# Kernel tuning notes

Measured on AMD Instinct MI355X. Metric: run time of the kernel, lower is better.

## Reference

```python
import math
import jax, jax.numpy as jnp
import numpy as np

B, T, D, H = 1, 4096, 1024, 16
HD = D // H  # 64

def setup_inputs() -> dict:
    key = jax.random.key(0)
    k1, k2, k3 = jax.random.split(key, 3)
    x = jax.random.normal(k1, (B, T, D), dtype=jnp.float32)
    # torch nn.Linear weight layout: [out_features, in_features]
    w_attn = jax.random.normal(k2, (3 * D, D), dtype=jnp.float32) * (1.0 / math.sqrt(D))
    w_proj = jax.random.normal(k3, (D, D), dtype=jnp.float32) * (1.0 / math.sqrt(D))
    return {"x": x, "w_attn": w_attn, "w_proj": w_proj}

def reference(x, w_attn, w_proj):
    b, t, d = x.shape
    qkv = jnp.einsum('btd,ed->bte', x, w_attn)  # [B,T,3D]
    q, k, v = jnp.split(qkv, 3, axis=-1)
    # [B,H,T,HD]
    q = q.reshape(b, t, H, HD).transpose(0, 2, 1, 3)
    k = k.reshape(b, t, H, HD).transpose(0, 2, 1, 3)
    v = v.reshape(b, t, H, HD).transpose(0, 2, 1, 3)
    scale = 1.0 / math.sqrt(HD)
    att = jnp.einsum('bhqd,bhkd->bhqk', q, k) * scale  # [B,H,T,T]
    causal = jnp.tril(jnp.ones((t, t), dtype=bool))
    att = jnp.where(causal[None, None], att, -jnp.inf)
    att = jax.nn.softmax(att, axis=-1)
    y = jnp.einsum('bhqk,bhkd->bhqd', att, v)  # [B,H,T,HD]
    y = y.transpose(0, 2, 1, 3).reshape(b, t, d)
    return jnp.einsum('btd,ed->bte', y, w_proj)
```

## Files before the change

### kernel.cpp

```cpp
#include <hip/hip_runtime.h>
#include <hip/hip_bf16.h>

typedef __bf16 bf16x8 __attribute__((ext_vector_type(8)));
typedef float  f32x4  __attribute__((ext_vector_type(4)));
typedef short  sh4    __attribute__((ext_vector_type(4)));

__device__ __forceinline__ void async_load16(const void* g, void* l) {
    __builtin_amdgcn_global_load_lds(
        (const __attribute__((address_space(1))) unsigned int*)g,
        (__attribute__((address_space(3))) unsigned int*)l,
        16, 0, 0);
}

__device__ __forceinline__ bool sniff_is_bf16(const void* src) {
    const unsigned int* p = (const unsigned int*)src;
    unsigned v = p[threadIdx.x & 63];
    unsigned e = (v >> 7) & 0xFF;
    unsigned long long m = __ballot(e >= 100 && e <= 140);
    return __popcll(m) >= 48;
}

__global__ __launch_bounds__(256) void to_bf16(const void* __restrict__ src,
                                               __bf16* __restrict__ dst, int n) {
    bool b16 = sniff_is_bf16(src);
    int i = (blockIdx.x * 256 + threadIdx.x) * 4;
    if (i >= n) return;
    if (b16) {
        *(uint2*)(dst + i) = *(const uint2*)((const __bf16*)src + i);
    } else {
        float4 v = *(const float4*)((const float*)src + i);
        dst[i]     = (__bf16)v.x;
        dst[i + 1] = (__bf16)v.y;
        dst[i + 2] = (__bf16)v.z;
        dst[i + 3] = (__bf16)v.w;
    }
}

__global__ __launch_bounds__(256) void gemm_bt(
    const __bf16* __restrict__ A,
    const __bf16* __restrict__ B,
    void* __restrict__ Cv,
    int M, int N, int K,
    const void* sniff)
{
    bool out_b16 = true;
    if (sniff) out_b16 = sniff_is_bf16(sniff);

    __shared__ __bf16 As[3 * 128 * 32];
    __shared__ __bf16 Bs[3 * 128 * 32];

    const int nwg = gridDim.x;
    const int cpx = nwg >> 3;
    const int sid = (blockIdx.x & 7) * cpx + (blockIdx.x >> 3);
    const int nbx = N >> 7;
    const int bx  = sid % nbx;
    const int by  = sid / nbx;

    const int tid  = threadIdx.x;
    const int lane = tid & 63;
    const int w    = tid >> 6;
    const int wm   = w >> 1, wn = w & 1;
    const int m0   = by * 128;
    const int n0   = bx * 128;
    const int c    = lane & 15;
    const int g    = lane >> 4;

    f32x4 acc[4][4] = {};

    const int e0 = tid * 8;
    const int e1 = e0 + 2048;
    const int r0 = e0 >> 5, c0 = e0 & 31;
    const int r1 = e1 >> 5, c1 = e1 & 31;

    const __bf16* a0 = A + (size_t)(m0 + r0) * K + c0;
    const __bf16* a1 = A + (size_t)(m0 + r1) * K + c1;
    const __bf16* b0 = B + (size_t)(n0 + r0) * K + c0;
    const __bf16* b1 = B + (size_t)(n0 + r1) * K + c1;

    const int KT = K >> 5;

    async_load16(a0, As + e0);
    async_load16(a1, As + e1);
    async_load16(b0, Bs + e0);
    async_load16(b1, Bs + e1);
    async_load16(a0 + 32, As + 4096 + e0);
    async_load16(a1 + 32, As + 4096 + e1);
    async_load16(b0 + 32, Bs + 4096 + e0);
    async_load16(b1 + 32, Bs + 4096 + e1);

    int cb = 0, sb = 2;
    for (int kt = 0; kt < KT; ++kt) {
        if (kt + 1 < KT) asm volatile("s_waitcnt vmcnt(4)" ::: "memory");
        else             asm volatile("s_waitcnt vmcnt(0)" ::: "memory");
        __builtin_amdgcn_s_barrier();
        asm volatile("" ::: "memory");

        if (kt + 2 < KT) {
            const int k0 = (kt + 2) << 5;
            async_load16(a0 + k0, As + sb * 4096 + e0);
            async_load16(a1 + k0, As + sb * 4096 + e1);
            async_load16(b0 + k0, Bs + sb * 4096 + e0);
            async_load16(b1 + k0, Bs + sb * 4096 + e1);
        }

        const __bf16* as_ = As + cb * 4096;
        const __bf16* bs_ = Bs + cb * 4096;

        bf16x8 af[4], bfr[4];
        #pragma unroll
        for (int i = 0; i < 4; i++)
            af[i] = *(const bf16x8*)&as_[(wm * 64 + i * 16 + c) * 32 + g * 8];
        #pragma unroll
        for (int j = 0; j < 4; j++)
            bfr[j] = *(const bf16x8*)&bs_[(wn * 64 + j * 16 + c) * 32 + g * 8];
        #pragma unroll
        for (int i = 0; i < 4; i++)
            #pragma unroll
            for (int j = 0; j < 4; j++)
                acc[i][j] = __builtin_amdgcn_mfma_f32_16x16x32_bf16(af[i], bfr[j], acc[i][j], 0, 0, 0);

        cb = (cb == 2) ? 0 : cb + 1;
        sb = (sb == 2) ? 0 : sb + 1;
    }

    #pragma unroll
    for (int i = 0; i < 4; i++) {
        const int row0 = m0 + wm * 64 + i * 16 + g * 4;
        #pragma unroll
        for (int j = 0; j < 4; j++) {
            const int col = n0 + wn * 64 + j * 16 + c;
            #pragma unroll
            for (int r = 0; r < 4; r++) {
                const size_t idx = (size_t)(row0 + r) * N + col;
                if (out_b16) ((__bf16*)Cv)[idx] = (__bf16)acc[i][j][r];
                else         ((float*)Cv)[idx]  = acc[i][j][r];
            }
        }
    }
}

__global__ __launch_bounds__(256) void gemm_bt64(
    const __bf16* __restrict__ A,
    const __bf16* __restrict__ B,
    void* __restrict__ Cv,
    int M, int N, int K,
    const void* sniff)
{
    bool out_b16 = true;
    if (sniff) out_b16 = sniff_is_bf16(sniff);

    __shared__ __bf16 As[3 * 128 * 32];
    __shared__ __bf16 Bs[3 * 64 * 32];

    const int nwg = gridDim.x;
    const int cpx = nwg >> 3;
    const int sid = (blockIdx.x & 7) * cpx + (blockIdx.x >> 3);
    const int nbx = N >> 6;
    const int bx  = sid % nbx;
    const int by  = sid / nbx;

    const int tid  = threadIdx.x;
    const int lane = tid & 63;
    const int w    = tid >> 6;
    const int wm   = w >> 1, wn = w & 1;
    const int m0   = by * 128;
    const int n0   = bx * 64;
    const int c    = lane & 15;
    const int g    = lane >> 4;

    f32x4 acc[4][2] = {};

    const int e0 = tid * 8;
    const int e1 = e0 + 2048;
    const int r0 = e0 >> 5, c0 = e0 & 31;
    const int r1 = e1 >> 5, c1 = e1 & 31;
    const int rb = tid >> 2, cbk = (tid & 3) * 8;

    const __bf16* a0 = A + (size_t)(m0 + r0) * K + c0;
    const __bf16* a1 = A + (size_t)(m0 + r1) * K + c1;
    const __bf16* bp = B + (size_t)(n0 + rb) * K + cbk;

    const int KT = K >> 5;

    async_load16(a0, As + e0);
    async_load16(a1, As + e1);
    async_load16(bp, Bs + e0);
    async_load16(a0 + 32, As + 4096 + e0);
    async_load16(a1 + 32, As + 4096 + e1);
    async_load16(bp + 32, Bs + 2048 + e0);

    int cb = 0, sb = 2;
    for (int kt = 0; kt < KT; ++kt) {
        if (kt + 1 < KT) asm volatile("s_waitcnt vmcnt(3)" ::: "memory");
        else             asm volatile("s_waitcnt vmcnt(0)" ::: "memory");
        __builtin_amdgcn_s_barrier();
        asm volatile("" ::: "memory");

        if (kt + 2 < KT) {
            const int k0 = (kt + 2) << 5;
            async_load16(a0 + k0, As + sb * 4096 + e0);
            async_load16(a1 + k0, As + sb * 4096 + e1);
            async_load16(bp + k0, Bs + sb * 2048 + e0);
        }

        const __bf16* as_ = As + cb * 4096;
        const __bf16* bs_ = Bs + cb * 2048;

        bf16x8 af[4], bfr[2];
        #pragma unroll
        for (int i = 0; i < 4; i++)
            af[i] = *(const bf16x8*)&as_[(wm * 64 + i * 16 + c) * 32 + g * 8];
        #pragma unroll
        for (int j = 0; j < 2; j++)
            bfr[j] = *(const bf16x8*)&bs_[(wn * 32 + j * 16 + c) * 32 + g * 8];
        #pragma unroll
        for (int i = 0; i < 4; i++)
            #pragma unroll
            for (int j = 0; j < 2; j++)
                acc[i][j] = __builtin_amdgcn_mfma_f32_16x16x32_bf16(af[i], bfr[j], acc[i][j], 0, 0, 0);

        cb = (cb == 2) ? 0 : cb + 1;
        sb = (sb == 2) ? 0 : sb + 1;
    }

    #pragma unroll
    for (int i = 0; i < 4; i++) {
        const int row0 = m0 + wm * 64 + i * 16 + g * 4;
        #pragma unroll
        for (int j = 0; j < 2; j++) {
            const int col = n0 + wn * 32 + j * 16 + c;
            #pragma unroll
            for (int r = 0; r < 4; r++) {
                const size_t idx = (size_t)(row0 + r) * N + col;
                if (out_b16) ((__bf16*)Cv)[idx] = (__bf16)acc[i][j][r];
                else         ((float*)Cv)[idx]  = acc[i][j][r];
            }
        }
    }
}

__global__ __launch_bounds__(256) void vtrans(const __bf16* __restrict__ qkv,
                                              __bf16* __restrict__ vT) {
    __shared__ __bf16 Lt[64 * 72];
    const int tid = threadIdx.x;
    const int h   = blockIdx.y;
    const int t0  = blockIdx.x * 64;
    #pragma unroll
    for (int rr = 0; rr < 2; rr++) {
        int e = rr * 2048 + tid * 8;
        int tr = e >> 6, tc = e & 63;
        bf16x8 v = *(const bf16x8*)&qkv[(size_t)(t0 + tr) * 3072 + 2048 + h * 64 + tc];
        #pragma unroll
        for (int i = 0; i < 8; i++) Lt[(tc + i) * 72 + tr] = v[i];
    }
    __syncthreads();
    #pragma unroll
    for (int rr = 0; rr < 2; rr++) {
        int e = rr * 2048 + tid * 8;
        int dr = e >> 6, dc = e & 63;
        *(bf16x8*)&vT[(size_t)h * 262144 + (size_t)dr * 4096 + t0 + dc]
            = *(const bf16x8*)&Lt[dr * 72 + dc];
    }
}

__global__ __launch_bounds__(512, 4) void attn_fwd(
    const __bf16* __restrict__ qkv,
    const __bf16* __restrict__ vT,
    __bf16* __restrict__ y)
{
    constexpr int LDQ = 3072;
    constexpr float SCL = 0.18033688011112042f;

    __shared__ __align__(16) char raw[50176];
    __bf16* ksb = (__bf16*)raw;
    __bf16* vsb = (__bf16*)(raw + 24576);
    float*  ls  = (float*)(raw + 49152);
    float*  F   = (float*)raw;

    const int id   = blockIdx.x;
    const int h    = (id & 7) * 2 + (id >> 8);
    const int pr   = (id >> 3) & 31;
    const int tid  = threadIdx.x;
    const int lane = tid & 63;
    const int w    = tid >> 6;
    const int kw   = w & 3;
    const int qw   = w >> 2;
    const int c    = lane & 15;
    const int g    = lane >> 4;
    const int qoff = h * 64;

    const int sr = tid >> 3, sg = ((tid & 7) ^ (sr & 7)) * 8;
    const __bf16* vbase = vT + (size_t)h * 262144;

    sh4 ones;
    #pragma unroll
    for (int i = 0; i < 4; i++) ones[i] = (short)0x3F80;

    const int qts[2] = {63 - pr, pr};

    #pragma unroll 1
    for (int ph = 0; ph < 2; ph++) {
        const int qt  = qts[ph];
        const int qs  = qt * 64;
        const int nkt = qt + 1;

        __syncthreads();

        async_load16(qkv + (size_t)sr * LDQ + 1024 + qoff + sg, ksb + tid * 8);
        async_load16(vbase + (size_t)sr * 4096 + sg, vsb + tid * 8);
        if (nkt > 1) {
            async_load16(qkv + (size_t)(64 + sr) * LDQ + 1024 + qoff + sg, ksb + 4096 + tid * 8);
            async_load16(vbase + (size_t)sr * 4096 + 64 + sg, vsb + 4096 + tid * 8);
        }

        bf16x8 qf[2][2];
        #pragma unroll
        for (int n = 0; n < 2; n++) {
            const __bf16* qrow = qkv + (size_t)(qs + qw * 32 + n * 16 + c) * LDQ + qoff;
            bf16x8 q0 = *(const bf16x8*)(qrow + g * 8);
            bf16x8 q1 = *(const bf16x8*)(qrow + 32 + g * 8);
            #pragma unroll
            for (int i = 0; i < 8; i++) {
                qf[n][0][i] = (__bf16)((float)q0[i] * SCL);
                qf[n][1][i] = (__bf16)((float)q1[i] * SCL);
            }
        }

        f32x4 ol[2] = {};
        f32x4 o[4][2] = {};

        for (int t = 0; t < nkt; t++) {
            if (t + 1 < nkt) asm volatile("s_waitcnt vmcnt(2)" ::: "memory");
            else             asm volatile("s_waitcnt vmcnt(0)" ::: "memory");
            __builtin_amdgcn_s_barrier();
            asm volatile("" ::: "memory");

            if (t + 2 < nkt) {
                const int nks = (t + 2) * 64;
                const int nb  = (t + 2) % 3;
                async_load16(qkv + (size_t)(nks + sr) * LDQ + 1024 + qoff + sg, ksb + (nb * 4096 + tid * 8));
                async_load16(vbase + (size_t)sr * 4096 + nks + sg, vsb + (nb * 4096 + tid * 8));
            }

            const __bf16* ks_ = ksb + (t % 3) * 4096;
            const __bf16* vs_ = vsb + (t % 3) * 4096;

            f32x4 sa[2] = {};
            #pragma unroll
            for (int s = 0; s < 2; s++) {
                bf16x8 kf = *(const bf16x8*)&ks_[(kw * 16 + c) * 64 + ((s * 4 + g) ^ (c & 7)) * 8];
                #pragma unroll
                for (int n = 0; n < 2; n++)
                    sa[n] = __builtin_amdgcn_mfma_f32_16x16x32_bf16(kf, qf[n][s], sa[n], 0, 0, 0);
            }

            if (t == nkt - 1) {
                #pragma unroll
                for (int n = 0; n < 2; n++)
                    #pragma unroll
                    for (int r = 0; r < 4; r++)
                        if (kw * 16 + g * 4 + r > qw * 32 + n * 16 + c) sa[n][r] = -1e30f;
            }

            sh4 vf[4];
            #pragma unroll
            for (int j = 0; j < 4; j++)
                vf[j] = *(const sh4*)&vs_[(j * 16 + c) * 64 + ((2 * kw + (g >> 1)) ^ (c & 7)) * 8 + (g & 1) * 4];

            #pragma unroll
            for (int n = 0; n < 2; n++) {
                __bf16 pb[4] __attribute__((aligned(8)));
                #pragma unroll
                for (int r = 0; r < 4; r++)
                    pb[r] = (__bf16)__builtin_amdgcn_exp2f(sa[n][r]);
                sh4 pbs = *(const sh4*)pb;
                ol[n] = __builtin_amdgcn_mfma_f32_16x16x16bf16_1k(ones, pbs, ol[n], 0, 0, 0);
                #pragma unroll
                for (int j = 0; j < 4; j++)
                    o[j][n] = __builtin_amdgcn_mfma_f32_16x16x16bf16_1k(vf[j], pbs, o[j][n], 0, 0, 0);
            }
        }

        __syncthreads();
        if (g == 0) {
            #pragma unroll
            for (int n = 0; n < 2; n++) ls[(kw * 4 + qw * 2 + n) * 16 + c] = ol[n][0];
        }
        __syncthreads();
        float rl = 0.f;
        if (w < 4) {
            float l_run = ls[(0 * 4 + w) * 16 + c] + ls[(1 * 4 + w) * 16 + c]
                        + ls[(2 * 4 + w) * 16 + c] + ls[(3 * 4 + w) * 16 + c];
            rl = 1.0f / l_run;
        }

        #pragma unroll
        for (int j = 0; j < 4; j++) {
            __syncthreads();
            #pragma unroll
            for (int n = 0; n < 2; n++)
                *(f32x4*)&F[((kw * 64) + (qw * 32 + n * 16 + c)) * 20 + g * 4] = o[j][n];
            __syncthreads();
            if (w < 4) {
                f32x4 t0 = *(const f32x4*)&F[((0 * 64) + (w * 16 + c)) * 20 + g * 4];
                f32x4 t1 = *(const f32x4*)&F[((1 * 64) + (w * 16 + c)) * 20 + g * 4];
                f32x4 t2 = *(const f32x4*)&F[((2 * 64) + (w * 16 + c)) * 20 + g * 4];
                f32x4 t3 = *(const f32x4*)&F[((3 * 64) + (w * 16 + c)) * 20 + g * 4];
                f32x4 tt = t0 + t1 + t2 + t3;
                __bf16 ob[4] __attribute__((aligned(8)));
                #pragma unroll
                for (int r = 0; r < 4; r++) ob[r] = (__bf16)(tt[r] * rl);
                *(uint2*)&y[(size_t)(qs + w * 16 + c) * 1024 + qoff + j * 16 + g * 4]
                    = *(const uint2*)ob;
            }
        }
    }
}

extern "C" void kernel_launch(void* const* d_in, const int* in_sizes, int n_in,
                              void* d_out, int out_size, void* d_ws, size_t ws_size,
                              hipStream_t stream) {
    constexpr int T = 4096, D = 1024;

    __bf16* cx   = (__bf16*)d_ws;
    __bf16* cwa  = cx  + (size_t)T * D;
    __bf16* cwp  = cwa + (size_t)3 * D * D;
    __bf16* qkv  = cwp + (size_t)D * D;
    __bf16* y    = qkv + (size_t)T * 3 * D;
    __bf16* vT   = cx;

    to_bf16<<<T * D / 1024, 256, 0, stream>>>(d_in[0], cx, T * D);
    to_bf16<<<3 * D * D / 1024, 256, 0, stream>>>(d_in[1], cwa, 3 * D * D);
    to_bf16<<<D * D / 1024, 256, 0, stream>>>(d_in[2], cwp, D * D);

    gemm_bt<<<(3 * D / 128) * (T / 128), 256, 0, stream>>>(cx, cwa, qkv, T, 3 * D, D, nullptr);
    vtrans<<<dim3(T / 64, 16), 256, 0, stream>>>(qkv, vT);
    attn_fwd<<<512, 512, 0, stream>>>(qkv, vT, y);
    gemm_bt64<<<(D / 64) * (T / 128), 256, 0, stream>>>(y, cwp, d_out, T, D, D, d_in[2]);
}
```

Before: 198.5 us.

## Fuse V transpose into QKV GEMM epilogue and merge bf16 conversion launches

The three input conversion launches become one kernel that picks its source by block index. The separate V-transpose kernel is removed. QKV GEMM blocks covering the V columns now transpose their tile through shared memory and write V^T directly, while Q/K go to a narrower 2048-stride buffer. This saves two kernel launches and a full read/write of V, at the cost of extra syncs and shared-memory traffic in the GEMM epilogue for a third of its blocks.

```diff
diff --git a/kernel.cpp b/kernel.cpp
--- a/kernel.cpp
+++ b/kernel.cpp
@@ -20,11 +20,16 @@
     return __popcll(m) >= 48;
 }
 
-__global__ __launch_bounds__(256) void to_bf16(const void* __restrict__ src,
-                                               __bf16* __restrict__ dst, int n) {
+__global__ __launch_bounds__(256) void to_bf16_3(
+    const void* __restrict__ s0, const void* __restrict__ s1,
+    const void* __restrict__ s2, __bf16* __restrict__ dst0) {
+    const int b = blockIdx.x;
+    const void* src; __bf16* dst; int boff;
+    if (b < 4096)      { src = s0; dst = dst0;           boff = b; }
+    else if (b < 7168) { src = s1; dst = dst0 + 4194304; boff = b - 4096; }
+    else               { src = s2; dst = dst0 + 7340032; boff = b - 7168; }
     bool b16 = sniff_is_bf16(src);
-    int i = (blockIdx.x * 256 + threadIdx.x) * 4;
-    if (i >= n) return;
+    int i = boff * 1024 + threadIdx.x * 4;
     if (b16) {
         *(uint2*)(dst + i) = *(const uint2*)((const __bf16*)src + i);
     } else {
@@ -39,13 +44,10 @@
 __global__ __launch_bounds__(256) void gemm_bt(
     const __bf16* __restrict__ A,
     const __bf16* __restrict__ B,
-    void* __restrict__ Cv,
-    int M, int N, int K,
-    const void* sniff)
+    __bf16* __restrict__ C,
+    int M, int N, int K, int ldc,
+    __bf16* __restrict__ vTout)
 {
-    bool out_b16 = true;
-    if (sniff) out_b16 = sniff_is_bf16(sniff);
-
     __shared__ __bf16 As[3 * 128 * 32];
     __shared__ __bf16 Bs[3 * 128 * 32];
 
@@ -123,6 +125,37 @@
         sb = (sb == 2) ? 0 : sb + 1;
     }
 
+    if (vTout && n0 >= ldc) {
+        const int h0 = (n0 - ldc) >> 6;
+        __bf16* Lt = As;
+        __syncthreads();
+        #pragma unroll
+        for (int p = 0; p < 2; p++) {
+            if (wn == p) {
+                #pragma unroll
+                for (int i = 0; i < 4; i++)
+                    #pragma unroll
+                    for (int j = 0; j < 4; j++) {
+                        __bf16 tb[4] __attribute__((aligned(8)));
+                        #pragma unroll
+                        for (int r = 0; r < 4; r++) tb[r] = (__bf16)acc[i][j][r];
+                        *(uint2*)&Lt[(j * 16 + c) * 136 + wm * 64 + i * 16 + g * 4]
+                            = *(const uint2*)tb;
+                    }
+            }
+            __syncthreads();
+            {
+                const int dl = tid >> 2, t0 = (tid & 3) * 32;
+                __bf16* dst = vTout + (size_t)(h0 + p) * 262144 + (size_t)dl * 4096 + m0 + t0;
+                #pragma unroll
+                for (int k = 0; k < 4; k++)
+                    *(bf16x8*)(dst + k * 8) = *(const bf16x8*)&Lt[dl * 136 + t0 + k * 8];
+            }
+            __syncthreads();
+        }
+        return;
+    }
+
     #pragma unroll
     for (int i = 0; i < 4; i++) {
         const int row0 = m0 + wm * 64 + i * 16 + g * 4;
@@ -131,9 +164,8 @@
             const int col = n0 + wn * 64 + j * 16 + c;
             #pragma unroll
             for (int r = 0; r < 4; r++) {
-                const size_t idx = (size_t)(row0 + r) * N + col;
-                if (out_b16) ((__bf16*)Cv)[idx] = (__bf16)acc[i][j][r];
-                else         ((float*)Cv)[idx]  = acc[i][j][r];
+                const size_t idx = (size_t)(row0 + r) * ldc + col;
+                C[idx] = (__bf16)acc[i][j][r];
             }
         }
     }
@@ -239,36 +271,12 @@
     }
 }
 
-__global__ __launch_bounds__(256) void vtrans(const __bf16* __restrict__ qkv,
-                                              __bf16* __restrict__ vT) {
-    __shared__ __bf16 Lt[64 * 72];
-    const int tid = threadIdx.x;
-    const int h   = blockIdx.y;
-    const int t0  = blockIdx.x * 64;
-    #pragma unroll
-    for (int rr = 0; rr < 2; rr++) {
-        int e = rr * 2048 + tid * 8;
-        int tr = e >> 6, tc = e & 63;
-        bf16x8 v = *(const bf16x8*)&qkv[(size_t)(t0 + tr) * 3072 + 2048 + h * 64 + tc];
-        #pragma unroll
-        for (int i = 0; i < 8; i++) Lt[(tc + i) * 72 + tr] = v[i];
-    }
-    __syncthreads();
-    #pragma unroll
-    for (int rr = 0; rr < 2; rr++) {
-        int e = rr * 2048 + tid * 8;
-        int dr = e >> 6, dc = e & 63;
-        *(bf16x8*)&vT[(size_t)h * 262144 + (size_t)dr * 4096 + t0 + dc]
-            = *(const bf16x8*)&Lt[dr * 72 + dc];
-    }
-}
-
 __global__ __launch_bounds__(512, 4) void attn_fwd(
     const __bf16* __restrict__ qkv,
     const __bf16* __restrict__ vT,
     __bf16* __restrict__ y)
 {
-    constexpr int LDQ = 3072;
+    constexpr int LDQ = 2048;
     constexpr float SCL = 0.18033688011112042f;
 
     __shared__ __align__(16) char raw[50176];
@@ -426,15 +434,11 @@
     __bf16* cwa  = cx  + (size_t)T * D;
     __bf16* cwp  = cwa + (size_t)3 * D * D;
     __bf16* qkv  = cwp + (size_t)D * D;
-    __bf16* y    = qkv + (size_t)T * 3 * D;
-    __bf16* vT   = cx;
-
-    to_bf16<<<T * D / 1024, 256, 0, stream>>>(d_in[0], cx, T * D);
-    to_bf16<<<3 * D * D / 1024, 256, 0, stream>>>(d_in[1], cwa, 3 * D * D);
-    to_bf16<<<D * D / 1024, 256, 0, stream>>>(d_in[2], cwp, D * D);
-
-    gemm_bt<<<(3 * D / 128) * (T / 128), 256, 0, stream>>>(cx, cwa, qkv, T, 3 * D, D, nullptr);
-    vtrans<<<dim3(T / 64, 16), 256, 0, stream>>>(qkv, vT);
+    __bf16* vT   = qkv + (size_t)T * 2048;
+    __bf16* y    = vT  + (size_t)16 * 64 * T;
+
+    to_bf16_3<<<8192, 256, 0, stream>>>(d_in[0], d_in[1], d_in[2], cx);
+    gemm_bt<<<(3 * D / 128) * (T / 128), 256, 0, stream>>>(cx, cwa, qkv, T, 3 * D, D, 2048, vT);
     attn_fwd<<<512, 512, 0, stream>>>(qkv, vT, y);
     gemm_bt64<<<(D / 64) * (T / 128), 256, 0, stream>>>(y, cwp, d_out, T, D, D, d_in[2]);
 }
```

Result: faster. 190.1 us, median of 2 (-4.2%).
